# Kernel tuning notes

Hardware: AMD Instinct MI355X
Metric: run time of the kernel (lower is better)

## Reference

```python
import jax, jax.numpy as jnp
import numpy as np


def setup_inputs() -> dict:
    key = jax.random.key(0)
    ks = jax.random.split(key, 6)
    B_, S, D_in, D_out, R, E = 4, 2048, 2048, 2048, 64, 16
    x = jax.random.normal(ks[0], (B_, S, D_in), dtype=jnp.float32)
    W_base = jax.random.normal(ks[1], (D_out, D_in), dtype=jnp.float32) * (D_in ** -0.5)
    b_base = jax.random.normal(ks[2], (D_out,), dtype=jnp.float32) * 0.02
    # orthogonal rows, as get_orthogonal_matrix(reservoir_size, in_features)
    G = np.asarray(jax.random.normal(ks[3], (D_in, R), dtype=jnp.float32))
    Q, _ = np.linalg.qr(G)  # [D_in, R] orthonormal columns
    A = jnp.asarray(Q.T, dtype=jnp.float32)  # [R, D_in]
    # B initialized to zeros in the module; use small random so delta is nontrivial
    Bmat = jax.random.normal(ks[4], (E, D_out, R), dtype=jnp.float32) * 0.02
    W_router = jax.random.normal(ks[5], (E, D_in), dtype=jnp.float32) * 0.02
    return {"x": x, "W_base": W_base, "b_base": b_base, "A": A, "B": Bmat,
            "W_router": W_router, "top_k": 2}


def reference(x, W_base, b_base, A, B, W_router, top_k):
    E = W_router.shape[0]
    base_output = jnp.einsum('bsi,oi->bso', x, W_base) + b_base          # [B,S,D_out]
    res_hidden = jnp.einsum('bsi,ri->bsr', x, A)                          # [B,S,R]
    router_logits = jnp.einsum('bsi,ei->bse', x, W_router)                # [B,S,E]
    routing_weights = jax.nn.softmax(router_logits, axis=-1)
    if top_k > 0 and top_k < E:
        _, top_idx = jax.lax.top_k(routing_weights, top_k)                # [B,S,k]
        mask = jax.nn.one_hot(top_idx, E, dtype=routing_weights.dtype).sum(axis=-2)
        routing_weights = routing_weights * mask
        routing_weights = routing_weights / (routing_weights.sum(axis=-1, keepdims=True) + 1e-6)
    # contract experts+rank without materializing [B,S,E,D_out]
    h = jnp.einsum('bsr,bse->bser', res_hidden, routing_weights)          # [B,S,E,R] (small)
    delta = jnp.einsum('bser,edr->bsd', h, B)                             # [B,S,D_out]
    return base_output + delta
```

## Files before the change

kernel.cpp:

```cpp
#include <hip/hip_runtime.h>
#include <hip/hip_bf16.h>

#define D_IN  2048
#define D_OUT 2048
#define RNK   64
#define NE    16
#define KTOT  3072

typedef __attribute__((ext_vector_type(8))) short bf16x8;
typedef __attribute__((ext_vector_type(4))) float f32x4;

__device__ __forceinline__ void async_ld16(const void* g, void* l) {
    __builtin_amdgcn_global_load_lds(
        (const __attribute__((address_space(1))) void*)g,
        (__attribute__((address_space(3))) void*)l,
        16, 0, 0);
}

__global__ __launch_bounds__(384) void castwa_kernel(
    const float* __restrict__ Wb, const float* __restrict__ Bm,
    const float* __restrict__ A,
    __hip_bfloat16* __restrict__ Wc, __hip_bfloat16* __restrict__ Ab)
{
    const int c = threadIdx.x * 8;
    const float* src;
    __hip_bfloat16* dst;
    if (blockIdx.x < D_OUT) {
        const int n = blockIdx.x;
        if (c < D_IN) {
            src = Wb + (size_t)n * D_IN + c;
        } else {
            const int j = c - D_IN;
            const int e = j >> 6, r = j & 63;
            src = Bm + ((size_t)e * D_OUT + n) * RNK + r;
        }
        dst = Wc + (size_t)n * KTOT + c;
    } else {
        if (c >= D_IN) return;
        const int r = blockIdx.x - D_OUT;
        src = A + (size_t)r * D_IN + c;
        dst = Ab + (size_t)r * D_IN + c;
    }
    const float4 a = *(const float4*)src;
    const float4 b = *(const float4*)(src + 4);
    const float vv[8] = {a.x, a.y, a.z, a.w, b.x, b.y, b.z, b.w};
    union { bf16x8 v; __hip_bfloat16 h[8]; } u;
#pragma unroll
    for (int q = 0; q < 8; ++q) u.h[q] = __float2bfloat16(vv[q]);
    *(bf16x8*)dst = u.v;
}

__global__ __launch_bounds__(256) void prep_kernel(
    const float* __restrict__ x, const float* __restrict__ Wr,
    const int* __restrict__ topk_p, __hip_bfloat16* __restrict__ Xc,
    float* __restrict__ wfin)
{
    __shared__ __align__(16) float wr_lds[2][NE * 256];
    const int tid = threadIdx.x;
    const int wave = tid >> 6, lane = tid & 63;
    const int t0 = blockIdx.x * 8 + wave * 2;

    float acc[NE][2];
#pragma unroll
    for (int e = 0; e < NE; ++e) { acc[e][0] = 0.f; acc[e][1] = 0.f; }

    const float4* x4 = (const float4*)x;

    auto stage = [&](int buf, int i) {
#pragma unroll
        for (int j = 0; j < 4; ++j) {
            const int r = wave * 4 + j;
            async_ld16(Wr + (size_t)r * D_IN + i * 256 + lane * 4,
                       (void*)&wr_lds[buf][r * 256]);
        }
    };

    stage(0, 0);
    __syncthreads();

#pragma unroll
    for (int i = 0; i < 8; ++i) {
        if (i < 7) stage((i + 1) & 1, i + 1);

        float4 xv[2];
#pragma unroll
        for (int t = 0; t < 2; ++t) {
            xv[t] = x4[(size_t)(t0 + t) * 512 + i * 64 + lane];
            union { short4 v; __hip_bfloat16 h[4]; } u;
            u.h[0] = __float2bfloat16(xv[t].x); u.h[1] = __float2bfloat16(xv[t].y);
            u.h[2] = __float2bfloat16(xv[t].z); u.h[3] = __float2bfloat16(xv[t].w);
            *(short4*)(Xc + (size_t)(t0 + t) * KTOT + (i * 64 + lane) * 4) = u.v;
        }

        const float4* wr4 = (const float4*)wr_lds[i & 1];
#pragma unroll
        for (int e = 0; e < NE; ++e) {
            const float4 wv = wr4[e * 64 + lane];
#pragma unroll
            for (int t = 0; t < 2; ++t)
                acc[e][t] += xv[t].x * wv.x + xv[t].y * wv.y
                           + xv[t].z * wv.z + xv[t].w * wv.w;
        }
        __syncthreads();
    }

#pragma unroll
    for (int off = 32; off; off >>= 1)
#pragma unroll
        for (int e = 0; e < NE; ++e)
#pragma unroll
            for (int t = 0; t < 2; ++t)
                acc[e][t] += __shfl_xor(acc[e][t], off, 64);

    if (lane < 2) {
        const int tt = lane;
        const int k = topk_p[0];
        float m = -1e30f;
#pragma unroll
        for (int e = 0; e < NE; ++e) m = fmaxf(m, acc[e][tt]);
        float w[NE]; float ssum = 0.f;
#pragma unroll
        for (int e = 0; e < NE; ++e) { w[e] = __expf(acc[e][tt] - m); ssum += w[e]; }
        const float inv = 1.f / ssum;
#pragma unroll
        for (int e = 0; e < NE; ++e) w[e] *= inv;
        float* wfout = wfin + (size_t)(t0 + tt) * NE;
        if (k > 0 && k < NE) {
            int chosen[NE];
#pragma unroll
            for (int e = 0; e < NE; ++e) chosen[e] = 0;
            float ksum = 0.f;
            for (int it = 0; it < k; ++it) {
                int bi = 0; float bv = -1.f;
                for (int e = 0; e < NE; ++e)
                    if (!chosen[e] && w[e] > bv) { bv = w[e]; bi = e; }
                chosen[bi] = 1; ksum += bv;
            }
            const float rinv = 1.f / (ksum + 1e-6f);
            for (int e = 0; e < NE; ++e) wfout[e] = chosen[e] ? w[e] * rinv : 0.f;
        } else {
            for (int e = 0; e < NE; ++e) wfout[e] = w[e];
        }
    }
}

__global__ __launch_bounds__(256) void rhfused_kernel(
    __hip_bfloat16* Xc, const __hip_bfloat16* __restrict__ Ab,
    const float* __restrict__ wfin)
{
    __shared__ __align__(16) float red[4][16][64];
    __shared__ __align__(16) float wf[16 * 16];
    const int tid = threadIdx.x;
    const int wave = tid >> 6, lane = tid & 63;
    const int qm = lane & 15, quad = lane >> 4;
    const int t0 = blockIdx.x * 16;

    const __hip_bfloat16* xrow =
        Xc + (size_t)(t0 + qm) * KTOT + wave * 512 + quad * 8;
    const __hip_bfloat16* brow =
        Ab + (size_t)qm * D_IN + wave * 512 + quad * 8;

    f32x4 acc[4] = {};
#pragma unroll
    for (int s = 0; s < 8; ++s) {
        const bf16x8 a0 = *(const bf16x8*)(xrow);
        const bf16x8 a1 = *(const bf16x8*)(xrow + 32);
        bf16x8 b0[4], b1[4];
#pragma unroll
        for (int nf = 0; nf < 4; ++nf) {
            b0[nf] = *(const bf16x8*)(brow + (size_t)nf * 16 * D_IN);
            b1[nf] = *(const bf16x8*)(brow + (size_t)nf * 16 * D_IN + 32);
        }
        xrow += 64; brow += 64;
#pragma unroll
        for (int nf = 0; nf < 4; ++nf) {
            acc[nf] = __builtin_amdgcn_mfma_f32_16x16x32_bf16(a0, b0[nf], acc[nf], 0, 0, 0);
            acc[nf] = __builtin_amdgcn_mfma_f32_16x16x32_bf16(a1, b1[nf], acc[nf], 0, 0, 0);
        }
    }

#pragma unroll
    for (int nf = 0; nf < 4; ++nf)
#pragma unroll
        for (int r = 0; r < 4; ++r)
            red[wave][quad * 4 + r][nf * 16 + qm] = acc[nf][r];

    if (tid < 64)
        ((float4*)wf)[tid] = ((const float4*)(wfin + (size_t)t0 * NE))[tid];
    __syncthreads();

#pragma unroll
    for (int it = 0; it < 8; ++it) {
        const int s = it * 256 + tid;
        const int t = s >> 7;
        const int chunk = s & 127;
        const int e = chunk >> 3, r0 = (chunk & 7) * 8;
        const float w = wf[t * 16 + e];
        union { bf16x8 v; __hip_bfloat16 h[8]; } u;
#pragma unroll
        for (int q = 0; q < 8; ++q) {
            const float rh = red[0][t][r0 + q] + red[1][t][r0 + q]
                           + red[2][t][r0 + q] + red[3][t][r0 + q];
            u.h[q] = __float2bfloat16(w * rh);
        }
        *(bf16x8*)(Xc + (size_t)(t0 + t) * KTOT + D_IN + chunk * 8) = u.v;
    }
}

__global__ __launch_bounds__(256) void gemm_kernel(
    const __hip_bfloat16* __restrict__ Am,
    const __hip_bfloat16* __restrict__ Bm,
    const float* __restrict__ bias,
    float* __restrict__ C, int M, int N)
{
    __shared__ __hip_bfloat16 lds_a[128 * 64];
    __shared__ __hip_bfloat16 lds_b[128 * 64];
    const int tid = threadIdx.x;
    const int wave = tid >> 6, lane = tid & 63;
    const int bm = blockIdx.x, bn = blockIdx.y;
    const int qm = lane & 15, quad = lane >> 4;
    const int ar = lane >> 3;
    const int ac = ((lane & 7) ^ ar) * 8;

    f32x4 acc[4][4] = {};
    const int wm = (wave >> 1) * 64, wn = (wave & 1) * 64;

    const __hip_bfloat16* ga[4];
    const __hip_bfloat16* gb[4];
#pragma unroll
    for (int j = 0; j < 4; ++j) {
        ga[j] = Am + (size_t)(bm * 128 + wave * 32 + j * 8 + ar) * KTOT + ac;
        gb[j] = Bm + (size_t)(bn * 128 + wave * 32 + j * 8 + ar) * KTOT + ac;
    }

    for (int k0 = 0; k0 < KTOT; k0 += 64) {
#pragma unroll
        for (int j = 0; j < 4; ++j) {
            async_ld16(ga[j], (void*)&lds_a[(wave * 4 + j) * 512]);
            async_ld16(gb[j], (void*)&lds_b[(wave * 4 + j) * 512]);
            ga[j] += 64; gb[j] += 64;
        }
        __syncthreads();

#pragma unroll
        for (int kk = 0; kk < 64; kk += 32) {
            const int cg = (kk >> 3) + quad;
            const int sw = (cg ^ (qm & 7)) * 8;
            bf16x8 af[4], bfr[4];
#pragma unroll
            for (int i = 0; i < 4; ++i)
                af[i] = *(const bf16x8*)&lds_a[(wm + i * 16 + qm) * 64 + sw];
#pragma unroll
            for (int j = 0; j < 4; ++j)
                bfr[j] = *(const bf16x8*)&lds_b[(wn + j * 16 + qm) * 64 + sw];
#pragma unroll
            for (int i = 0; i < 4; ++i)
#pragma unroll
                for (int j = 0; j < 4; ++j)
                    acc[i][j] = __builtin_amdgcn_mfma_f32_16x16x32_bf16(
                        af[i], bfr[j], acc[i][j], 0, 0, 0);
        }
        __syncthreads();
    }

    const size_t row0 = (size_t)bm * 128 + wm;
    const int col0 = bn * 128 + wn;
#pragma unroll
    for (int j = 0; j < 4; ++j) {
        const int col = col0 + j * 16 + qm;
        const float bb = bias[col];
#pragma unroll
        for (int i = 0; i < 4; ++i) {
#pragma unroll
            for (int r = 0; r < 4; ++r) {
                const size_t row = row0 + i * 16 + quad * 4 + r;
                C[row * (size_t)N + col] = acc[i][j][r] + bb;
            }
        }
    }
}

extern "C" void kernel_launch(void* const* d_in, const int* in_sizes, int n_in,
                              void* d_out, int out_size, void* d_ws, size_t ws_size,
                              hipStream_t stream) {
    const float* x    = (const float*)d_in[0];
    const float* Wb   = (const float*)d_in[1];
    const float* bb   = (const float*)d_in[2];
    const float* A    = (const float*)d_in[3];
    const float* Bm   = (const float*)d_in[4];
    const float* Wr   = (const float*)d_in[5];
    const int*   topk = (const int*)d_in[6];
    float* out = (float*)d_out;
    const int T = in_sizes[0] / D_IN;

    __hip_bfloat16* Xc = (__hip_bfloat16*)d_ws;
    __hip_bfloat16* Wc = (__hip_bfloat16*)((char*)d_ws + (size_t)T * KTOT * 2);
    __hip_bfloat16* Ab = (__hip_bfloat16*)d_out;
    float* wfin = (float*)d_out + 8 * 1024 * 1024;

    castwa_kernel<<<D_OUT + RNK, 384, 0, stream>>>(Wb, Bm, A, Wc, Ab);
    prep_kernel<<<T / 8, 256, 0, stream>>>(x, Wr, topk, Xc, wfin);
    rhfused_kernel<<<T / 16, 256, 0, stream>>>(Xc, Ab, wfin);
    gemm_kernel<<<dim3(T / 128, D_OUT / 128), 256, 0, stream>>>(Xc, Wc, bb, out, T, D_OUT);
}
```

Measured before the change: 305.7 us.

## Fuse router prep and reservoir projection into one kernel using LDS-staged x tile

Merges the routing/softmax/top-k prep kernel with the reservoir-hidden MFMA kernel into a single 512-thread kernel handling 16 tokens per block. The bf16 copy of x is kept in a swizzled LDS buffer so the A-projection reads it from shared memory instead of re-reading Xc from global, and routing weights stay in LDS rather than round-tripping through global memory. This removes one launch and an intermediate global pass. In exchange it uses 80KB of LDS per block, which lowers occupancy, and adds an extra block-wide sync per chunk.

```diff
diff --git a/kernel.cpp b/kernel.cpp
--- a/kernel.cpp
+++ b/kernel.cpp
@@ -50,68 +50,72 @@
     *(bf16x8*)dst = u.v;
 }
 
-__global__ __launch_bounds__(256) void prep_kernel(
+__global__ __launch_bounds__(512) void prep2_kernel(
     const float* __restrict__ x, const float* __restrict__ Wr,
-    const int* __restrict__ topk_p, __hip_bfloat16* __restrict__ Xc,
-    float* __restrict__ wfin)
+    const __hip_bfloat16* __restrict__ Ab,
+    const int* __restrict__ topk_p, __hip_bfloat16* __restrict__ Xc)
 {
-    __shared__ __align__(16) float wr_lds[2][NE * 256];
+    __shared__ __align__(16) char smem[81920];
+    __hip_bfloat16* xb = (__hip_bfloat16*)smem;
+    float* stage = (float*)(smem + 65536);
+    float* red = (float*)smem;
+    float* wf  = (float*)(smem + 65536);
+
     const int tid = threadIdx.x;
     const int wave = tid >> 6, lane = tid & 63;
-    const int t0 = blockIdx.x * 8 + wave * 2;
+    const int qm = lane & 15, quad = lane >> 4;
+    const int t0 = blockIdx.x * 16;
+    const int tA = t0 + wave * 2;
 
     float acc[NE][2];
 #pragma unroll
     for (int e = 0; e < NE; ++e) { acc[e][0] = 0.f; acc[e][1] = 0.f; }
 
     const float4* x4 = (const float4*)x;
-
-    auto stage = [&](int buf, int i) {
-#pragma unroll
-        for (int j = 0; j < 4; ++j) {
-            const int r = wave * 4 + j;
-            async_ld16(Wr + (size_t)r * D_IN + i * 256 + lane * 4,
-                       (void*)&wr_lds[buf][r * 256]);
-        }
-    };
-
-    stage(0, 0);
-    __syncthreads();
-
-#pragma unroll
-    for (int i = 0; i < 8; ++i) {
-        if (i < 7) stage((i + 1) & 1, i + 1);
-
-        float4 xv[2];
+    float4 xv[2], xn[2];
+    xv[0] = x4[(size_t)tA * 512 + lane];
+    xv[1] = x4[(size_t)(tA + 1) * 512 + lane];
+
+    for (int c = 0; c < 8; ++c) {
+        async_ld16(Wr + (size_t)wave * D_IN + c * 256 + lane * 4,
+                   (void*)(stage + wave * 256));
+        async_ld16(Wr + (size_t)(wave + 8) * D_IN + c * 256 + lane * 4,
+                   (void*)(stage + (wave + 8) * 256));
+        if (c < 7) {
+            xn[0] = x4[(size_t)tA * 512 + (c + 1) * 64 + lane];
+            xn[1] = x4[(size_t)(tA + 1) * 512 + (c + 1) * 64 + lane];
+        }
+        __syncthreads();
+
 #pragma unroll
         for (int t = 0; t < 2; ++t) {
-            xv[t] = x4[(size_t)(t0 + t) * 512 + i * 64 + lane];
+            const int tl = wave * 2 + t;
             union { short4 v; __hip_bfloat16 h[4]; } u;
             u.h[0] = __float2bfloat16(xv[t].x); u.h[1] = __float2bfloat16(xv[t].y);
             u.h[2] = __float2bfloat16(xv[t].z); u.h[3] = __float2bfloat16(xv[t].w);
-            *(short4*)(Xc + (size_t)(t0 + t) * KTOT + (i * 64 + lane) * 4) = u.v;
-        }
-
-        const float4* wr4 = (const float4*)wr_lds[i & 1];
+            *(short4*)(Xc + (size_t)(t0 + tl) * KTOT + c * 256 + lane * 4) = u.v;
+            const int gg = c * 32 + (lane >> 1);
+            const int pg = gg ^ (tl & 7);
+            *(short4*)((char*)xb + tl * 4096 + pg * 16 + (lane & 1) * 8) = u.v;
+        }
+        const float4* wr4 = (const float4*)stage;
 #pragma unroll
         for (int e = 0; e < NE; ++e) {
             const float4 wv = wr4[e * 64 + lane];
-#pragma unroll
-            for (int t = 0; t < 2; ++t)
-                acc[e][t] += xv[t].x * wv.x + xv[t].y * wv.y
-                           + xv[t].z * wv.z + xv[t].w * wv.w;
-        }
-        __syncthreads();
+            acc[e][0] += xv[0].x*wv.x + xv[0].y*wv.y + xv[0].z*wv.z + xv[0].w*wv.w;
+            acc[e][1] += xv[1].x*wv.x + xv[1].y*wv.y + xv[1].z*wv.z + xv[1].w*wv.w;
+        }
+        __syncthreads();
+        if (c < 7) { xv[0] = xn[0]; xv[1] = xn[1]; }
     }
 
 #pragma unroll
     for (int off = 32; off; off >>= 1)
 #pragma unroll
-        for (int e = 0; e < NE; ++e)
-#pragma unroll
-            for (int t = 0; t < 2; ++t)
-                acc[e][t] += __shfl_xor(acc[e][t], off, 64);
-
+        for (int e = 0; e < NE; ++e) {
+            acc[e][0] += __shfl_xor(acc[e][0], off, 64);
+            acc[e][1] += __shfl_xor(acc[e][1], off, 64);
+        }
     if (lane < 2) {
         const int tt = lane;
         const int k = topk_p[0];
@@ -124,7 +128,7 @@
         const float inv = 1.f / ssum;
 #pragma unroll
         for (int e = 0; e < NE; ++e) w[e] *= inv;
-        float* wfout = wfin + (size_t)(t0 + tt) * NE;
+        float* wfout = wf + (size_t)(wave * 2 + tt) * NE;
         if (k > 0 && k < NE) {
             int chosen[NE];
 #pragma unroll
@@ -142,67 +146,57 @@
             for (int e = 0; e < NE; ++e) wfout[e] = w[e];
         }
     }
-}
-
-__global__ __launch_bounds__(256) void rhfused_kernel(
-    __hip_bfloat16* Xc, const __hip_bfloat16* __restrict__ Ab,
-    const float* __restrict__ wfin)
-{
-    __shared__ __align__(16) float red[4][16][64];
-    __shared__ __align__(16) float wf[16 * 16];
-    const int tid = threadIdx.x;
-    const int wave = tid >> 6, lane = tid & 63;
-    const int qm = lane & 15, quad = lane >> 4;
-    const int t0 = blockIdx.x * 16;
-
-    const __hip_bfloat16* xrow =
-        Xc + (size_t)(t0 + qm) * KTOT + wave * 512 + quad * 8;
-    const __hip_bfloat16* brow =
-        Ab + (size_t)qm * D_IN + wave * 512 + quad * 8;
-
-    f32x4 acc[4] = {};
-#pragma unroll
-    for (int s = 0; s < 8; ++s) {
-        const bf16x8 a0 = *(const bf16x8*)(xrow);
-        const bf16x8 a1 = *(const bf16x8*)(xrow + 32);
+
+    f32x4 racc[4] = {};
+    const int kb = wave * 256;
+#pragma unroll
+    for (int s = 0; s < 4; ++s) {
+        const int k0 = kb + s * 64;
+        const int gg0 = (k0 >> 3) + quad;
+        const bf16x8 a0 = *(const bf16x8*)((char*)xb + qm * 4096 + ((gg0 ^ (qm & 7)) * 16));
+        const bf16x8 a1 = *(const bf16x8*)((char*)xb + qm * 4096 + (((gg0 + 4) ^ (qm & 7)) * 16));
         bf16x8 b0[4], b1[4];
 #pragma unroll
         for (int nf = 0; nf < 4; ++nf) {
-            b0[nf] = *(const bf16x8*)(brow + (size_t)nf * 16 * D_IN);
-            b1[nf] = *(const bf16x8*)(brow + (size_t)nf * 16 * D_IN + 32);
-        }
-        xrow += 64; brow += 64;
+            const __hip_bfloat16* bp = Ab + (size_t)(qm + nf * 16) * D_IN + k0 + quad * 8;
+            b0[nf] = *(const bf16x8*)bp;
+            b1[nf] = *(const bf16x8*)(bp + 32);
+        }
 #pragma unroll
         for (int nf = 0; nf < 4; ++nf) {
-            acc[nf] = __builtin_amdgcn_mfma_f32_16x16x32_bf16(a0, b0[nf], acc[nf], 0, 0, 0);
-            acc[nf] = __builtin_amdgcn_mfma_f32_16x16x32_bf16(a1, b1[nf], acc[nf], 0, 0, 0);
-        }
-    }
+            racc[nf] = __builtin_amdgcn_mfma_f32_16x16x32_bf16(a0, b0[nf], racc[nf], 0, 0, 0);
+            racc[nf] = __builtin_amdgcn_mfma_f32_16x16x32_bf16(a1, b1[nf], racc[nf], 0, 0, 0);
+        }
+    }
+    __syncthreads();
 
 #pragma unroll
     for (int nf = 0; nf < 4; ++nf)
 #pragma unroll
         for (int r = 0; r < 4; ++r)
-            red[wave][quad * 4 + r][nf * 16 + qm] = acc[nf][r];
-
-    if (tid < 64)
-        ((float4*)wf)[tid] = ((const float4*)(wfin + (size_t)t0 * NE))[tid];
+            red[(wave * 16 + quad * 4 + r) * 64 + nf * 16 + qm] = racc[nf][r];
     __syncthreads();
 
 #pragma unroll
-    for (int it = 0; it < 8; ++it) {
-        const int s = it * 256 + tid;
+    for (int it = 0; it < 4; ++it) {
+        const int s = it * 512 + tid;
         const int t = s >> 7;
         const int chunk = s & 127;
         const int e = chunk >> 3, r0 = (chunk & 7) * 8;
-        const float w = wf[t * 16 + e];
+        const float wgt = wf[t * 16 + e];
+        float4 s0 = {0.f, 0.f, 0.f, 0.f}, s1 = {0.f, 0.f, 0.f, 0.f};
+#pragma unroll
+        for (int w2 = 0; w2 < 8; ++w2) {
+            const float4 p0 = ((const float4*)red)[(w2 * 16 + t) * 16 + (r0 >> 2)];
+            const float4 p1 = ((const float4*)red)[(w2 * 16 + t) * 16 + (r0 >> 2) + 1];
+            s0.x += p0.x; s0.y += p0.y; s0.z += p0.z; s0.w += p0.w;
+            s1.x += p1.x; s1.y += p1.y; s1.z += p1.z; s1.w += p1.w;
+        }
         union { bf16x8 v; __hip_bfloat16 h[8]; } u;
-#pragma unroll
-        for (int q = 0; q < 8; ++q) {
-            const float rh = red[0][t][r0 + q] + red[1][t][r0 + q]
-                           + red[2][t][r0 + q] + red[3][t][r0 + q];
-            u.h[q] = __float2bfloat16(w * rh);
-        }
+        u.h[0] = __float2bfloat16(wgt * s0.x); u.h[1] = __float2bfloat16(wgt * s0.y);
+        u.h[2] = __float2bfloat16(wgt * s0.z); u.h[3] = __float2bfloat16(wgt * s0.w);
+        u.h[4] = __float2bfloat16(wgt * s1.x); u.h[5] = __float2bfloat16(wgt * s1.y);
+        u.h[6] = __float2bfloat16(wgt * s1.z); u.h[7] = __float2bfloat16(wgt * s1.w);
         *(bf16x8*)(Xc + (size_t)(t0 + t) * KTOT + D_IN + chunk * 8) = u.v;
     }
 }
@@ -296,10 +290,8 @@
     __hip_bfloat16* Xc = (__hip_bfloat16*)d_ws;
     __hip_bfloat16* Wc = (__hip_bfloat16*)((char*)d_ws + (size_t)T * KTOT * 2);
     __hip_bfloat16* Ab = (__hip_bfloat16*)d_out;
-    float* wfin = (float*)d_out + 8 * 1024 * 1024;
 
     castwa_kernel<<<D_OUT + RNK, 384, 0, stream>>>(Wb, Bm, A, Wc, Ab);
-    prep_kernel<<<T / 8, 256, 0, stream>>>(x, Wr, topk, Xc, wfin);
-    rhfused_kernel<<<T / 16, 256, 0, stream>>>(Xc, Ab, wfin);
+    prep2_kernel<<<T / 16, 512, 0, stream>>>(x, Wr, Ab, topk, Xc);
     gemm_kernel<<<dim3(T / 128, D_OUT / 128), 256, 0, stream>>>(Xc, Wc, bb, out, T, D_OUT);
 }
```

Result: faster. 278.5 us (-8.9%).
